# Kernel tuning notes

Measured on AMD Instinct MI355X. Metric: run time of the kernel, lower is better.

The kernel has to match this reference:

```python
import math
import jax, jax.numpy as jnp
import numpy as np

N_HEAD = 16

def setup_inputs() -> dict:
    key = jax.random.key(0)
    ks = jax.random.split(key, 3)
    B, T, C = 2, 2048, 1024
    x = jax.random.normal(ks[0], (B, T, C), dtype=jnp.float32)
    W_kqv = jax.random.normal(ks[1], (3 * C, C), dtype=jnp.float32) * 0.02
    b_kqv = jnp.zeros((3 * C,), dtype=jnp.float32)
    W_proj = jax.random.normal(ks[2], (C, C), dtype=jnp.float32) * 0.02
    b_proj = jnp.zeros((C,), dtype=jnp.float32)
    return {"x": x, "W_kqv": W_kqv, "b_kqv": b_kqv, "W_proj": W_proj, "b_proj": b_proj}

def reference(x, W_kqv, b_kqv, W_proj, b_proj):
    B, T, C = x.shape
    nh = N_HEAD
    hd = C // nh
    # fused QKV projection, then view [B,T,nh,3*hd] and slice into k,q,v
    kqv = (x @ W_kqv.T + b_kqv).reshape(B, T, nh, 3, hd)
    k = kqv[..., 0, :]  # [B,T,nh,hd]
    q = kqv[..., 1, :]
    v = kqv[..., 2, :]
    scale = 1.0 / math.sqrt(hd)
    att = jnp.einsum("bthd,bshd->bhts", q, k) * scale  # [B,nh,T,T]
    causal = jnp.tril(jnp.ones((T, T), dtype=bool))
    att = jnp.where(causal[None, None], att, -jnp.inf)
    att = jax.nn.softmax(att, axis=-1)
    y = jnp.einsum("bhts,bshd->bthd", att, v).reshape(B, T, C)
    return y @ W_proj.T + b_proj
```

## Files before the change

kernel.cpp:

```cpp
#include <hip/hip_runtime.h>

#define TSEQ 2048
#define NHEAD 16
#define HD 64
#define CDIM 1024
#define BT 4096

typedef unsigned short u16;
typedef __bf16 bf16x8 __attribute__((ext_vector_type(8)));
typedef float f32x4 __attribute__((ext_vector_type(4)));
typedef float f32x16 __attribute__((ext_vector_type(16)));

union Frag {
  int4 i4;
  bf16x8 b;
  u16 u[8];
};

__device__ __forceinline__ u16 f2b(float f) {
  union { float f; unsigned u; } x;
  x.f = f;
  unsigned r = x.u + 0x7fffu + ((x.u >> 16) & 1u);
  return (u16)(r >> 16);
}

#define N4X 1048576
#define N4W1 786432
#define N4W2 262144
__global__ void cvt3_kernel(const float* __restrict__ x, const float* __restrict__ w1,
                            const float* __restrict__ w2, u16* __restrict__ ox,
                            u16* __restrict__ o1, u16* __restrict__ o2) {
  int i = blockIdx.x * blockDim.x + threadIdx.x;
  int stride = gridDim.x * blockDim.x;
  for (int idx = i; idx < N4X + N4W1 + N4W2; idx += stride) {
    const float4* src;
    ushort4* dst;
    int k;
    if (idx < N4X) { src = (const float4*)x; dst = (ushort4*)ox; k = idx; }
    else if (idx < N4X + N4W1) { src = (const float4*)w1; dst = (ushort4*)o1; k = idx - N4X; }
    else { src = (const float4*)w2; dst = (ushort4*)o2; k = idx - N4X - N4W1; }
    float4 f = src[k];
    ushort4 o;
    o.x = f2b(f.x); o.y = f2b(f.y); o.z = f2b(f.z); o.w = f2b(f.w);
    dst[k] = o;
  }
}

__device__ __forceinline__ void gload_lds16(const u16* g, u16* l) {
  __builtin_amdgcn_global_load_lds((__attribute__((address_space(1))) void*)g,
                                   (__attribute__((address_space(3))) void*)l, 16, 0, 0);
}

__device__ __forceinline__ void gemm_tiles(const u16* __restrict__ A, const u16* __restrict__ Bw,
                                           int K, int m0, int n0,
                                           u16 (*__restrict__ Ash)[128 * 32],
                                           u16 (*__restrict__ Bsh)[128 * 32],
                                           f32x4 acc[4][4]) {
  const int tid = threadIdx.x;
  const int lane = tid & 63;
  const int w = tid >> 6;
  const int wr = (w >> 1) * 64, wc = (w & 1) * 64;
  const int lr = lane & 15;
  const int hi = lane >> 4;
  const int r0 = tid >> 2;
  const int cS = ((tid & 3) ^ ((tid >> 3) & 3)) << 3;
  const int frg = (hi ^ ((lr >> 1) & 3)) << 3;

#define GSTAGE(B, KO)                                                                 \
  { _Pragma("unroll") for (int s = 0; s < 2; s++) {                                   \
      gload_lds16(&A[(size_t)(m0 + s * 64 + r0) * K + (KO) + cS], &Ash[B][(s * 256 + tid) * 8]); \
      gload_lds16(&Bw[(size_t)(n0 + s * 64 + r0) * K + (KO) + cS], &Bsh[B][(s * 256 + tid) * 8]); \
  } }

  GSTAGE(0, 0)
  int cur = 0;
  for (int k0 = 0; k0 < K; k0 += 32) {
    __syncthreads();
    Frag af[4], bfr[4];
#pragma unroll
    for (int i = 0; i < 4; i++) {
      af[i].i4 = *(const int4*)&Ash[cur][(wr + i * 16 + lr) * 32 + frg];
      bfr[i].i4 = *(const int4*)&Bsh[cur][(wc + i * 16 + lr) * 32 + frg];
    }
    __builtin_amdgcn_sched_barrier(0);
    if (k0 + 32 < K) GSTAGE(cur ^ 1, k0 + 32)
    __builtin_amdgcn_sched_barrier(0);
#pragma unroll
    for (int mf = 0; mf < 4; mf++)
#pragma unroll
      for (int nf = 0; nf < 4; nf++)
        acc[mf][nf] = __builtin_amdgcn_mfma_f32_16x16x32_bf16(af[mf].b, bfr[nf].b, acc[mf][nf], 0, 0, 0);
    cur ^= 1;
  }
#undef GSTAGE
}

__global__ __launch_bounds__(256) void gemm_kqv(const u16* __restrict__ xb, const u16* __restrict__ wb,
                                                const float* __restrict__ bias,
                                                u16* __restrict__ qb, u16* __restrict__ kb,
                                                u16* __restrict__ vtb) {
  __shared__ __align__(16) u16 SMEMU[16384];
  u16 (*Ash)[4096] = (u16(*)[4096])&SMEMU[0];
  u16 (*Bsh)[4096] = (u16(*)[4096])&SMEMU[8192];
  const int m0 = blockIdx.y * 128, n0 = blockIdx.x * 128;
  f32x4 acc[4][4];
#pragma unroll
  for (int i = 0; i < 4; i++)
#pragma unroll
    for (int j = 0; j < 4; j++) acc[i][j] = (f32x4){0.f, 0.f, 0.f, 0.f};

  gemm_tiles(xb, wb, CDIM, m0, n0, Ash, Bsh, acc);

  const int tid = threadIdx.x;
  const int lane = tid & 63;
  const int w = tid >> 6;
  const int wr = (w >> 1) * 64, wc = (w & 1) * 64;
  const int lr = lane & 15;
  const int rbase = (lane >> 4) << 2;

  __syncthreads();
  u16* Csh = SMEMU;
#pragma unroll
  for (int mf = 0; mf < 4; mf++) {
#pragma unroll
    for (int nf = 0; nf < 4; nf++) {
      f32x4 a = acc[mf][nf];
      int nl = wc + nf * 16 + lr;
      int n = n0 + nl;
      float bval = bias[n];
      int sres = ((n0 + wc + nf * 16) % 192) >> 6;
      float scale = (sres == 1) ? 0.125f : 1.f;
#pragma unroll
      for (int r = 0; r < 4; r++) {
        int ml = wr + mf * 16 + rbase + r;
        Csh[ml * 128 + (nl ^ (((ml >> 2) & 3) << 4))] = f2b((a[r] + bval) * scale);
      }
    }
  }
  __syncthreads();

  const int bb = m0 >> 11, tt = m0 & 2047;
#pragma unroll
  for (int j = 0; j < 2; j++) {
    int ns = n0 + j * 64;
    int h = ns / 192;
    int sres = (ns % 192) >> 6;
    int bh2 = (bb << 4) + h;
    if (sres == 2) {
      int ch = tid & 15;
      int d0 = tid >> 4;
#pragma unroll
      for (int it = 0; it < 4; it++) {
        int d = d0 + it * 16;
        unsigned pk[4];
#pragma unroll
        for (int p = 0; p < 4; p++) {
          int c0 = ch * 8 + p * 2;
          int g0 = c0 >> 6, c6a = c0 & 63;
          int mA = g0 * 64 + ((c6a & 51) | ((c6a & 8) >> 1) | ((c6a & 4) << 1));
          int c1 = c0 + 1;
          int g1 = c1 >> 6, c6b = c1 & 63;
          int mB = g1 * 64 + ((c6b & 51) | ((c6b & 8) >> 1) | ((c6b & 4) << 1));
          unsigned lo = Csh[mA * 128 + ((j * 64 + d) ^ (((mA >> 2) & 3) << 4))];
          unsigned hi2 = Csh[mB * 128 + ((j * 64 + d) ^ (((mB >> 2) & 3) << 4))];
          pk[p] = lo | (hi2 << 16);
        }
        int4 v4; v4.x = pk[0]; v4.y = pk[1]; v4.z = pk[2]; v4.w = pk[3];
        *(int4*)&vtb[((size_t)bh2 * HD + d) * TSEQ + tt + ch * 8] = v4;
      }
    } else {
      u16* dst = (sres == 0) ? kb : qb;
      int ch = tid & 7;
      int rg = tid >> 3;
#pragma unroll
      for (int it = 0; it < 4; it++) {
        int m = rg + it * 32;
        int ccp = (j * 8 + ch) ^ (((m >> 2) & 3) << 1);
        int4 v4 = *(const int4*)&Csh[m * 128 + (ccp << 3)];
        *(int4*)&dst[((size_t)bh2 * TSEQ + tt + m) * HD + ch * 8] = v4;
      }
    }
  }
}

__device__ __forceinline__ void gemm_tiles64(const u16* __restrict__ A, const u16* __restrict__ Bw,
                                             int K, int m0, int n0,
                                             u16 (*__restrict__ Ash)[2048],
                                             u16 (*__restrict__ Bsh)[4096],
                                             f32x4 acc[2][4]) {
  const int tid = threadIdx.x;
  const int lane = tid & 63;
  const int w = tid >> 6;
  const int wr = (w >> 1) * 32, wc = (w & 1) * 64;
  const int lr = lane & 15;
  const int hi = lane >> 4;
  const int r0 = tid >> 2;
  const int cS = ((tid & 3) ^ ((tid >> 3) & 3)) << 3;
  const int frg = (hi ^ ((lr >> 1) & 3)) << 3;

#define GSTAGE64(B, KO)                                                               \
  {                                                                                   \
    gload_lds16(&A[(size_t)(m0 + r0) * K + (KO) + cS], &Ash[B][tid * 8]);             \
    _Pragma("unroll") for (int s = 0; s < 2; s++)                                     \
      gload_lds16(&Bw[(size_t)(n0 + s * 64 + r0) * K + (KO) + cS], &Bsh[B][(s * 256 + tid) * 8]); \
  }

  GSTAGE64(0, 0)
  int cur = 0;
  for (int k0 = 0; k0 < K; k0 += 32) {
    __syncthreads();
    Frag af[2], bfr[4];
#pragma unroll
    for (int i = 0; i < 2; i++)
      af[i].i4 = *(const int4*)&Ash[cur][(wr + i * 16 + lr) * 32 + frg];
#pragma unroll
    for (int i = 0; i < 4; i++)
      bfr[i].i4 = *(const int4*)&Bsh[cur][(wc + i * 16 + lr) * 32 + frg];
    __builtin_amdgcn_sched_barrier(0);
    if (k0 + 32 < K) GSTAGE64(cur ^ 1, k0 + 32)
    __builtin_amdgcn_sched_barrier(0);
#pragma unroll
    for (int mf = 0; mf < 2; mf++)
#pragma unroll
      for (int nf = 0; nf < 4; nf++)
        acc[mf][nf] = __builtin_amdgcn_mfma_f32_16x16x32_bf16(af[mf].b, bfr[nf].b, acc[mf][nf], 0, 0, 0);
    cur ^= 1;
  }
#undef GSTAGE64
}

__global__ __launch_bounds__(256) void gemm_proj(const u16* __restrict__ yb, const u16* __restrict__ wb,
                                                 const float* __restrict__ bias,
                                                 float* __restrict__ out) {
  __shared__ __align__(16) u16 Ash[2][2048];
  __shared__ __align__(16) u16 Bsh[2][4096];
  const int m0 = blockIdx.y * 64, n0 = blockIdx.x * 128;
  f32x4 acc[2][4];
#pragma unroll
  for (int i = 0; i < 2; i++)
#pragma unroll
    for (int j = 0; j < 4; j++) acc[i][j] = (f32x4){0.f, 0.f, 0.f, 0.f};

  gemm_tiles64(yb, wb, CDIM, m0, n0, Ash, Bsh, acc);

  const int tid = threadIdx.x;
  const int lane = tid & 63;
  const int w = tid >> 6;
  const int wr = (w >> 1) * 32, wc = (w & 1) * 64;
  const int lr = lane & 15;
  const int rbase = (lane >> 4) << 2;
#pragma unroll
  for (int mf = 0; mf < 2; mf++) {
#pragma unroll
    for (int nf = 0; nf < 4; nf++) {
      f32x4 a = acc[mf][nf];
      int n = n0 + wc + nf * 16 + lr;
      float bval = bias[n];
#pragma unroll
      for (int r = 0; r < 4; r++) {
        int m = m0 + wr + mf * 16 + rbase + r;
        out[(size_t)m * CDIM + n] = a[r] + bval;
      }
    }
  }
}

__global__ __launch_bounds__(256, 2) void attn_kernel(const u16* __restrict__ qb,
                                                      const u16* __restrict__ kb,
                                                      const u16* __restrict__ vtb,
                                                      u16* __restrict__ yb) {
  __shared__ u16 Ksh[2][128 * 64];
  __shared__ u16 Vsh[2][64 * 128];

  const int tid = threadIdx.x;
  const int lane = tid & 63;
  const int w = tid >> 6;
  const int l31 = lane & 31;
  const int hi32 = lane >> 5;
  const int swz = l31 & 7;

  const int jj = blockIdx.x;
  const int bh = jj & 31;
  const int cls = jj >> 5;
  const int qbk = (cls < 8) ? (15 - cls) : (cls - 8);
  const int q0w = qbk * 128 + w * 32;
  const int LN = qbk + 1;

  const u16* Qp = qb + (size_t)bh * TSEQ * HD;
  const u16* Kp = kb + (size_t)bh * TSEQ * HD;
  const u16* Vt = vtb + (size_t)bh * HD * TSEQ;

  Frag qf[4];
#pragma unroll
  for (int k = 0; k < 4; k++)
    qf[k].i4 = *(const int4*)&Qp[(size_t)(q0w + l31) * HD + k * 16 + hi32 * 8];

  f32x16 O0, O1;
  float lp = 0.f;
#pragma unroll
  for (int i = 0; i < 16; i++) { O0[i] = 0.f; O1[i] = 0.f; }

#define STAGE(B, JT)                                                                 \
  {                                                                                  \
    const int kvb = (JT) * 128;                                                      \
    _Pragma("unroll") for (int p = 0; p < 4; p++) {                                  \
      int c = tid + p * 256;                                                         \
      int row = c >> 3, c16 = c & 7;                                                 \
      gload_lds16(&Kp[(size_t)(kvb + row) * HD + ((c16 ^ (row & 7)) << 3)],          \
                  &Ksh[B][c * 8]);                                                   \
    }                                                                                \
    _Pragma("unroll") for (int p = 0; p < 4; p++) {                                  \
      int c = tid + p * 256;                                                         \
      int row = c >> 4, c16 = c & 15;                                                \
      int gofs = ((c16 >> 3) << 6) + (((c16 & 7) ^ (row & 7)) << 3);                 \
      gload_lds16(&Vt[(size_t)row * TSEQ + kvb + gofs], &Vsh[B][c * 8]);             \
    }                                                                                \
  }

#define PACK2(dst, SV, base)                                                         \
    asm("v_cvt_pk_bf16_f32 %0, %1, %2" : "=v"(dst.i4.x) : "v"(SV[base + 0]), "v"(SV[base + 1])); \
    asm("v_cvt_pk_bf16_f32 %0, %1, %2" : "=v"(dst.i4.y) : "v"(SV[base + 2]), "v"(SV[base + 3])); \
    asm("v_cvt_pk_bf16_f32 %0, %1, %2" : "=v"(dst.i4.z) : "v"(SV[base + 4]), "v"(SV[base + 5])); \
    asm("v_cvt_pk_bf16_f32 %0, %1, %2" : "=v"(dst.i4.w) : "v"(SV[base + 6]), "v"(SV[base + 7]));

  STAGE(0, 0)
  int cur = 0;
  for (int jt = 0; jt < LN; ++jt) {
    __syncthreads();
    const bool diag = (jt == LN - 1);
    const int wlim = diag ? w : 3;
    const u16* Kt = Ksh[cur];
    const u16* Vl = Vsh[cur];

    Frag ka[4][4], vA[4][2], vB[4][2];
#pragma unroll
    for (int sh = 0; sh < 4; ++sh) {
      if (sh <= wlim) {
#pragma unroll
        for (int k = 0; k < 4; ++k)
          ka[sh][k].i4 = *(const int4*)&Kt[(sh * 32 + l31) * 64 + (((2 * k + hi32) ^ swz) << 3)];
#pragma unroll
        for (int k = 0; k < 2; ++k) {
          int cofs = ((sh >> 1) << 6) + (((((sh & 1) << 2) + 2 * k + hi32) ^ swz) << 3);
          vA[sh][k].i4 = *(const int4*)&Vl[l31 * 128 + cofs];
          vB[sh][k].i4 = *(const int4*)&Vl[(32 + l31) * 128 + cofs];
        }
      }
    }
    __builtin_amdgcn_sched_barrier(0);
    if (jt + 1 < LN) STAGE(cur ^ 1, jt + 1)
    __builtin_amdgcn_sched_barrier(0);
#pragma unroll
    for (int sh = 0; sh < 4; ++sh) {
      if (sh <= wlim) {
        f32x16 S;
#pragma unroll
        for (int i = 0; i < 16; i++) S[i] = 0.f;
        __builtin_amdgcn_s_setprio(1);
#pragma unroll
        for (int k = 0; k < 4; k++)
          S = __builtin_amdgcn_mfma_f32_32x32x16_bf16(ka[sh][k].b, qf[k].b, S, 0, 0, 0);
        __builtin_amdgcn_s_setprio(0);
        if (diag && sh == w) {
#pragma unroll
          for (int reg = 0; reg < 16; reg++) {
            int crow = (reg & 3) + 8 * (reg >> 2) + 4 * hi32;
            S[reg] = (crow <= l31) ? __expf(S[reg]) : 0.f;
          }
        } else {
#pragma unroll
          for (int reg = 0; reg < 16; reg++) S[reg] = __expf(S[reg]);
        }
#pragma unroll
        for (int reg = 0; reg < 16; reg++) lp += S[reg];
        Frag pa[2];
        PACK2(pa[0], S, 0)
        PACK2(pa[1], S, 8)
        __builtin_amdgcn_s_setprio(1);
#pragma unroll
        for (int k = 0; k < 2; k++) {
          O0 = __builtin_amdgcn_mfma_f32_32x32x16_bf16(pa[k].b, vA[sh][k].b, O0, 0, 0, 0);
          O1 = __builtin_amdgcn_mfma_f32_32x32x16_bf16(pa[k].b, vB[sh][k].b, O1, 0, 0, 0);
        }
        __builtin_amdgcn_s_setprio(0);
      }
    }
    cur ^= 1;
  }
#undef STAGE
#undef PACK2

  float lpt = lp + __shfl_xor(lp, 32);
  const int b = bh >> 4, h = bh & 15;
#pragma unroll
  for (int reg = 0; reg < 16; reg++) {
    int qlocal = (reg & 3) + 8 * (reg >> 2) + 4 * hi32;
    float invr = 1.f / __shfl(lpt, qlocal);
    int t = q0w + qlocal;
    size_t rowoff = ((size_t)(b * TSEQ + t) << 10) + (h << 6);
    yb[rowoff + l31] = f2b(O0[reg] * invr);
    yb[rowoff + 32 + l31] = f2b(O1[reg] * invr);
  }
}

extern "C" void kernel_launch(void* const* d_in, const int* in_sizes, int n_in,
                              void* d_out, int out_size, void* d_ws, size_t ws_size,
                              hipStream_t stream) {
  const float* x = (const float*)d_in[0];
  const float* Wkqv = (const float*)d_in[1];
  const float* bkqv = (const float*)d_in[2];
  const float* Wproj = (const float*)d_in[3];
  const float* bproj = (const float*)d_in[4];
  float* out = (float*)d_out;

  u16* ws = (u16*)d_ws;
  u16* xb = ws;
  u16* wkqvb = xb + 4194304;
  u16* wprojb = wkqvb + 3145728;
  u16* qb = wprojb + 1048576;
  u16* kb = qb + 4194304;
  u16* vtb = kb + 4194304;
  u16* yb = vtb + 4194304;

  cvt3_kernel<<<2048, 256, 0, stream>>>(x, Wkqv, Wproj, xb, wkqvb, wprojb);
  gemm_kqv<<<dim3(24, 32), 256, 0, stream>>>(xb, wkqvb, bkqv, qb, kb, vtb);
  attn_kernel<<<512, 256, 0, stream>>>(qb, kb, vtb, yb);
  gemm_proj<<<dim3(8, 64), 256, 0, stream>>>(yb, wprojb, bproj, out);
}
```

Baseline: 94.23 us.

## Enlarge QKV GEMM tiles to 256x256 with 512 threads and deeper pipeline

Rewrites the QKV projection GEMM to use 256x256 output tiles with 8 waves, each wave computing 128x64. The K loop now uses 64-wide double-buffered stages split into two 32-wide halves, with explicit vmcnt waits and raw s_barrier. MFMA sections run at raised wave priority via s_setprio. The aim is more data reuse per LDS load and better overlap of global loads with compute. The cost is a grid of only 192 blocks on a 256-CU device, and 128KB of LDS per block, which limits occupancy to one block per CU.

```diff
diff --git a/kernel.cpp b/kernel.cpp
--- a/kernel.cpp
+++ b/kernel.cpp
@@ -51,89 +51,93 @@
                                    (__attribute__((address_space(3))) void*)l, 16, 0, 0);
 }
 
-__device__ __forceinline__ void gemm_tiles(const u16* __restrict__ A, const u16* __restrict__ Bw,
-                                           int K, int m0, int n0,
-                                           u16 (*__restrict__ Ash)[128 * 32],
-                                           u16 (*__restrict__ Bsh)[128 * 32],
-                                           f32x4 acc[4][4]) {
+__global__ __launch_bounds__(512, 2) void gemm_kqv(const u16* __restrict__ xb, const u16* __restrict__ wb,
+                                                   const float* __restrict__ bias,
+                                                   u16* __restrict__ qb, u16* __restrict__ kb,
+                                                   u16* __restrict__ vtb) {
+  __shared__ __align__(16) u16 SM[65536];
+
   const int tid = threadIdx.x;
   const int lane = tid & 63;
-  const int w = tid >> 6;
-  const int wr = (w >> 1) * 64, wc = (w & 1) * 64;
+  const int wid = tid >> 6;
+  const int wr = wid >> 2;
+  const int wc = wid & 3;
   const int lr = lane & 15;
   const int hi = lane >> 4;
-  const int r0 = tid >> 2;
+  const int frg = (hi ^ ((lr >> 1) & 3)) << 3;
   const int cS = ((tid & 3) ^ ((tid >> 3) & 3)) << 3;
-  const int frg = (hi ^ ((lr >> 1) & 3)) << 3;
-
-#define GSTAGE(B, KO)                                                                 \
-  { _Pragma("unroll") for (int s = 0; s < 2; s++) {                                   \
-      gload_lds16(&A[(size_t)(m0 + s * 64 + r0) * K + (KO) + cS], &Ash[B][(s * 256 + tid) * 8]); \
-      gload_lds16(&Bw[(size_t)(n0 + s * 64 + r0) * K + (KO) + cS], &Bsh[B][(s * 256 + tid) * 8]); \
-  } }
-
-  GSTAGE(0, 0)
-  int cur = 0;
-  for (int k0 = 0; k0 < K; k0 += 32) {
-    __syncthreads();
-    Frag af[4], bfr[4];
-#pragma unroll
-    for (int i = 0; i < 4; i++) {
-      af[i].i4 = *(const int4*)&Ash[cur][(wr + i * 16 + lr) * 32 + frg];
-      bfr[i].i4 = *(const int4*)&Bsh[cur][(wc + i * 16 + lr) * 32 + frg];
-    }
-    __builtin_amdgcn_sched_barrier(0);
-    if (k0 + 32 < K) GSTAGE(cur ^ 1, k0 + 32)
-    __builtin_amdgcn_sched_barrier(0);
-#pragma unroll
-    for (int mf = 0; mf < 4; mf++)
+  const int srow = tid >> 2;
+
+  const int m0 = blockIdx.y * 256, n0 = blockIdx.x * 256;
+
+  f32x4 acc[8][4];
+#pragma unroll
+  for (int i = 0; i < 8; i++)
+#pragma unroll
+    for (int j = 0; j < 4; j++) acc[i][j] = (f32x4){0.f, 0.f, 0.f, 0.f};
+
+#define STG(b, jt, p)                                                                 \
+  {                                                                                   \
+    const size_t ko = (size_t)(jt) * 64 + (p) * 32;                                   \
+    u16* Ad = SM + (b) * 32768 + (p) * 8192;                                          \
+    u16* Bd = SM + (b) * 32768 + 16384 + (p) * 8192;                                  \
+    _Pragma("unroll") for (int s = 0; s < 2; s++)                                     \
+      gload_lds16(&xb[(size_t)(m0 + s * 128 + srow) * CDIM + ko + cS],                \
+                  &Ad[(s * 512 + tid) * 8]);                                          \
+    _Pragma("unroll") for (int s = 0; s < 2; s++)                                     \
+      gload_lds16(&wb[(size_t)(n0 + s * 128 + srow) * CDIM + ko + cS],                \
+                  &Bd[(s * 512 + tid) * 8]);                                          \
+  }
+
+  STG(0, 0, 0)
+  STG(0, 0, 1)
+  for (int jt = 0; jt < 16; ++jt) {
+    const int bsel = jt & 1;
+#pragma unroll
+    for (int p = 0; p < 2; ++p) {
+      if (jt == 15 && p == 1) asm volatile("s_waitcnt vmcnt(0)" ::: "memory");
+      else                    asm volatile("s_waitcnt vmcnt(4)" ::: "memory");
+      __builtin_amdgcn_s_barrier();
+      const u16* Ap = SM + bsel * 32768 + p * 8192;
+      const u16* Bp = SM + bsel * 32768 + 16384 + p * 8192;
+      Frag af[8], bf[4];
+#pragma unroll
+      for (int mf = 0; mf < 8; mf++)
+        af[mf].i4 = *(const int4*)&Ap[(wr * 128 + mf * 16 + lr) * 32 + frg];
 #pragma unroll
       for (int nf = 0; nf < 4; nf++)
-        acc[mf][nf] = __builtin_amdgcn_mfma_f32_16x16x32_bf16(af[mf].b, bfr[nf].b, acc[mf][nf], 0, 0, 0);
-    cur ^= 1;
-  }
-#undef GSTAGE
-}
-
-__global__ __launch_bounds__(256) void gemm_kqv(const u16* __restrict__ xb, const u16* __restrict__ wb,
-                                                const float* __restrict__ bias,
-                                                u16* __restrict__ qb, u16* __restrict__ kb,
-                                                u16* __restrict__ vtb) {
-  __shared__ __align__(16) u16 SMEMU[16384];
-  u16 (*Ash)[4096] = (u16(*)[4096])&SMEMU[0];
-  u16 (*Bsh)[4096] = (u16(*)[4096])&SMEMU[8192];
-  const int m0 = blockIdx.y * 128, n0 = blockIdx.x * 128;
-  f32x4 acc[4][4];
-#pragma unroll
-  for (int i = 0; i < 4; i++)
-#pragma unroll
-    for (int j = 0; j < 4; j++) acc[i][j] = (f32x4){0.f, 0.f, 0.f, 0.f};
-
-  gemm_tiles(xb, wb, CDIM, m0, n0, Ash, Bsh, acc);
-
-  const int tid = threadIdx.x;
-  const int lane = tid & 63;
-  const int w = tid >> 6;
-  const int wr = (w >> 1) * 64, wc = (w & 1) * 64;
-  const int lr = lane & 15;
-  const int rbase = (lane >> 4) << 2;
+        bf[nf].i4 = *(const int4*)&Bp[(wc * 64 + nf * 16 + lr) * 32 + frg];
+      __builtin_amdgcn_sched_barrier(0);
+      if (jt + 1 < 16) STG((jt + 1) & 1, jt + 1, p)
+      __builtin_amdgcn_sched_barrier(0);
+      __builtin_amdgcn_s_setprio(1);
+#pragma unroll
+      for (int mf = 0; mf < 8; mf++)
+#pragma unroll
+        for (int nf = 0; nf < 4; nf++)
+          acc[mf][nf] = __builtin_amdgcn_mfma_f32_16x16x32_bf16(af[mf].b, bf[nf].b, acc[mf][nf], 0, 0, 0);
+      __builtin_amdgcn_s_setprio(0);
+    }
+  }
+#undef STG
 
   __syncthreads();
-  u16* Csh = SMEMU;
-#pragma unroll
-  for (int mf = 0; mf < 4; mf++) {
+  u16* Csh = SM;
+  const int rbase = hi << 2;
+#pragma unroll
+  for (int mf = 0; mf < 8; mf++) {
 #pragma unroll
     for (int nf = 0; nf < 4; nf++) {
       f32x4 a = acc[mf][nf];
-      int nl = wc + nf * 16 + lr;
+      int nl = wc * 64 + nf * 16 + lr;
       int n = n0 + nl;
       float bval = bias[n];
-      int sres = ((n0 + wc + nf * 16) % 192) >> 6;
+      int sres = ((n0 + wc * 64 + nf * 16) % 192) >> 6;
       float scale = (sres == 1) ? 0.125f : 1.f;
 #pragma unroll
       for (int r = 0; r < 4; r++) {
-        int ml = wr + mf * 16 + rbase + r;
-        Csh[ml * 128 + (nl ^ (((ml >> 2) & 3) << 4))] = f2b((a[r] + bval) * scale);
+        int ml = wr * 128 + mf * 16 + rbase + r;
+        Csh[ml * 256 + (nl ^ (((ml >> 2) & 3) << 4))] = f2b((a[r] + bval) * scale);
       }
     }
   }
@@ -141,14 +145,14 @@
 
   const int bb = m0 >> 11, tt = m0 & 2047;
 #pragma unroll
-  for (int j = 0; j < 2; j++) {
+  for (int j = 0; j < 4; j++) {
     int ns = n0 + j * 64;
     int h = ns / 192;
     int sres = (ns % 192) >> 6;
     int bh2 = (bb << 4) + h;
     if (sres == 2) {
-      int ch = tid & 15;
-      int d0 = tid >> 4;
+      int ch = tid & 31;
+      int d0 = tid >> 5;
 #pragma unroll
       for (int it = 0; it < 4; it++) {
         int d = d0 + it * 16;
@@ -161,8 +165,8 @@
           int c1 = c0 + 1;
           int g1 = c1 >> 6, c6b = c1 & 63;
           int mB = g1 * 64 + ((c6b & 51) | ((c6b & 8) >> 1) | ((c6b & 4) << 1));
-          unsigned lo = Csh[mA * 128 + ((j * 64 + d) ^ (((mA >> 2) & 3) << 4))];
-          unsigned hi2 = Csh[mB * 128 + ((j * 64 + d) ^ (((mB >> 2) & 3) << 4))];
+          unsigned lo = Csh[mA * 256 + ((j * 64 + d) ^ (((mA >> 2) & 3) << 4))];
+          unsigned hi2 = Csh[mB * 256 + ((j * 64 + d) ^ (((mB >> 2) & 3) << 4))];
           pk[p] = lo | (hi2 << 16);
         }
         int4 v4; v4.x = pk[0]; v4.y = pk[1]; v4.z = pk[2]; v4.w = pk[3];
@@ -174,9 +178,9 @@
       int rg = tid >> 3;
 #pragma unroll
       for (int it = 0; it < 4; it++) {
-        int m = rg + it * 32;
+        int m = rg + it * 64;
         int ccp = (j * 8 + ch) ^ (((m >> 2) & 3) << 1);
-        int4 v4 = *(const int4*)&Csh[m * 128 + (ccp << 3)];
+        int4 v4 = *(const int4*)&Csh[m * 256 + (ccp << 3)];
         *(int4*)&dst[((size_t)bh2 * TSEQ + tt + m) * HD + ch * 8] = v4;
       }
     }
@@ -423,7 +427,7 @@
   u16* yb = vtb + 4194304;
 
   cvt3_kernel<<<2048, 256, 0, stream>>>(x, Wkqv, Wproj, xb, wkqvb, wprojb);
-  gemm_kqv<<<dim3(24, 32), 256, 0, stream>>>(xb, wkqvb, bkqv, qb, kb, vtb);
+  gemm_kqv<<<dim3(12, 16), 512, 0, stream>>>(xb, wkqvb, bkqv, qb, kb, vtb);
   attn_kernel<<<512, 256, 0, stream>>>(qb, kb, vtb, yb);
   gemm_proj<<<dim3(8, 64), 256, 0, stream>>>(yb, wprojb, bproj, out);
 }
```

After: 95.64 us. Within noise of the previous version (+1.5%).
